# Performance work log

Measured on AMD Instinct MI355X. Metric: run time of the kernel, lower is better.

## Reference

```python
import math
import jax, jax.numpy as jnp
import numpy as np
from jax import lax

# Fixed values for the module's random shift hyperparams (in their legal ranges)
S2, S3, S5, S6 = 2, 1, -1, 1  # p_2_1_0, p_3_1_0, p_5_1_1, p_6_1_0


def setup_inputs() -> dict:
    key = jax.random.key(0)
    k1, k2, k3, k4, k5 = jax.random.split(key, 5)
    n, c, h, w = 16, 112, 48, 48
    x = jax.random.normal(k1, (n, c, h, w), dtype=jnp.float32)
    bound7 = math.sqrt(3.0 / (w * 3))
    p7_w = jax.random.uniform(k2, (3, w), minval=-bound7, maxval=bound7, dtype=jnp.float32)
    p8_w = jax.random.normal(k3, (1, c, h, 1), dtype=jnp.float32) * 0.02
    p19_w = jax.random.normal(k4, (1, c, 1, 1), dtype=jnp.float32) * 0.02
    cb = 1.0 / math.sqrt(c * 3)
    conv_w = jax.random.uniform(k5, (c, c, 1, 3), minval=-cb, maxval=cb, dtype=jnp.float32)
    return {"x": x, "p7_w": p7_w, "p8_w": p8_w, "p19_w": p19_w, "conv_w": conv_w}


def reference(x, p7_w, p8_w, p19_w, conv_w):
    n, c, h, w = x.shape
    hw = h * w
    # t_1: unfold (1,3) dilation (1,3) pad (0,3) -> width shifts of {-3,0,+3}, zero padded
    xp = jnp.pad(x, ((0, 0), (0, 0), (0, 0), (3, 3)))
    t1 = jnp.stack([xp[..., 3 * k: 3 * k + w] for k in range(3)], axis=2)  # (n,c,3,h,w)
    t2 = jnp.roll(x, S2, axis=2)
    t3 = jnp.roll(t1, S3, axis=3)
    t4 = t3.mean(axis=1)                     # (n,3,h,w)
    t5 = jnp.roll(t2, S5, axis=3)
    t6 = jnp.roll(t4, S6, axis=2)
    t7 = jnp.einsum('nkhw,kw->nh', t6, p7_w)  # einsum 'abcd,bdef->aecf' collapsed -> (n,h)
    t8 = p8_w * t5
    t9 = x + t8
    t10 = t8 - t9                             # mathematically -x, kept as written
    # p_11: Conv2d(c,c,(1,3),dilation=(1,2),padding=(0,2)), width-preserving
    t11 = lax.conv_general_dilated(
        t10, conv_w, window_strides=(1, 1), padding=((0, 0), (2, 2)),
        rhs_dilation=(1, 2), dimension_numbers=('NCHW', 'OIHW', 'NCHW'))
    # t_12: unfold (7,1) dilation (2,1) pad (6,0) on t_7 viewed (n,1,h,1)
    t7p = jnp.pad(t7, ((0, 0), (6, 6)))
    t12 = jnp.stack([t7p[:, 2 * k: 2 * k + h] for k in range(7)], axis=1)  # (n,7,h)
    t13 = jnp.maximum(t11, x)
    # t_14 = bmm(x^T, t13)/sqrt(c): (n,hw,hw)
    t14 = jnp.einsum('ncp,ncq->npq', x.reshape(n, c, hw), t13.reshape(n, c, hw)) / math.sqrt(c)
    t15 = jnp.abs(t12)
    t17 = t15.mean(axis=2)                    # (n,7)
    t18 = (t17[:, None, :] - t10.reshape(n, c * h * w // 7, 7)).reshape(n, c, h, w)
    t19 = p19_w * t18
    # t_16 = t7 - t14 (broadcast over last h*w*w of row-block view), t_20 = t7 + t16
    t14r = t14.reshape(n, h, w * h * w)
    t7b = t7[:, :, None]
    t16 = t7b - t14r
    t20 = (t7b + t16).reshape(n, hw, hw)
    t21 = jnp.einsum('ncp,npq->ncq', t19.reshape(n, c, hw), t20) / math.sqrt(hw)
    return t21.reshape(n, c, h, w)
```

## Files before the change

### kernel.cpp

```cpp
#include <hip/hip_runtime.h>

typedef __attribute__((ext_vector_type(8))) short bfrag;
typedef __attribute__((ext_vector_type(4))) float f32x4;

namespace {
constexpr int N_ = 16, C_ = 112, H_ = 48, W_ = 48, HW_ = 2304;
constexpr int NKS = 18;
constexpr int WS_T7 = 0;
constexpr int WS_A = 1024;
constexpr int WS_WPACK = 40960;
constexpr int WS_GBF = 62464;
constexpr int WS_SPART = 177152;
}

__device__ __forceinline__ float f4e(const float4& v, int e) {
  return e == 0 ? v.x : e == 1 ? v.y : e == 2 ? v.z : v.w;
}
__device__ __forceinline__ unsigned short f2bf(float f) {
  unsigned u = __float_as_uint(f);
  return (unsigned short)((u + 0x7FFFu + ((u >> 16) & 1u)) >> 16);
}
__device__ __forceinline__ float bf2f(unsigned short s) {
  return __uint_as_float(((unsigned)s) << 16);
}

__global__ __launch_bounds__(192) void ath_t7(const float* __restrict__ x,
                                              const float* __restrict__ p7,
                                              float* __restrict__ ws) {
  const int h = blockIdx.x, n = blockIdx.y;
  const int tid = threadIdx.x;
  __shared__ float q[48];
  __shared__ float wred[3];
  if (tid < 48) {
    float s = 0.f;
#pragma unroll
    for (int k = 0; k < 3; ++k) {
      int wp = tid + 3 - 3 * k;
      if (wp >= 0 && wp < 48) s += p7[k * 48 + wp];
    }
    q[tid] = s;
  }
  __syncthreads();
  const int c16 = tid / 12, qq = tid - 12 * c16;
  const float qv0 = q[4 * qq], qv1 = q[4 * qq + 1];
  const float qv2 = q[4 * qq + 2], qv3 = q[4 * qq + 3];
  float d = 0.f;
#pragma unroll
  for (int p = 0; p < 7; ++p) {
    const int c = c16 + 16 * p;
    float4 v = *(const float4*)&x[((size_t)n * C_ + c) * HW_ + h * W_ + 4 * qq];
    d += v.x * qv0 + v.y * qv1 + v.z * qv2 + v.w * qv3;
  }
#pragma unroll
  for (int off = 32; off >= 1; off >>= 1) d += __shfl_xor(d, off);
  if ((tid & 63) == 0) wred[tid >> 6] = d;
  __syncthreads();
  if (tid == 0)
    ws[WS_T7 + n * H_ + (h + 2) % 48] =
        (wred[0] + wred[1] + wred[2]) * (1.0f / 112.0f);
}

__global__ __launch_bounds__(256) void ath_gram(const float* __restrict__ x,
                                                const float* __restrict__ cw,
                                                float* __restrict__ ws) {
  const int bid = blockIdx.x;
  const int tid = threadIdx.x;
  if (bid >= 2 * NKS * N_) {
    int idx = (bid - 2 * NKS * N_) * 256 + tid;
    if (idx < 3 * 112 * 32) {
      int kx = idx / (112 * 32);
      int r = idx - kx * 112 * 32;
      int o = r >> 5;
      int i0 = (r & 31) * 4;
      unsigned short v[4];
#pragma unroll
      for (int e = 0; e < 4; ++e) {
        int i = i0 + e;
        v[e] = (i < 112) ? f2bf(cw[o * 336 + i * 3 + kx]) : (unsigned short)0;
      }
      unsigned short* wp = (unsigned short*)(ws + WS_WPACK);
      *(ushort4*)&wp[(kx * 112 + o) * 128 + i0] = make_ushort4(v[0], v[1], v[2], v[3]);
    }
    return;
  }
  const int half = bid & 1;
  const int ks = (bid >> 1) % NKS;
  const int n = bid / (2 * NKS);
  const int k0 = ks * 128;
  const int lane = tid & 63, wv = tid >> 6;
  const int lr = lane & 15, lg = lane >> 4;
  __shared__ __align__(16) unsigned short As[112][136];
  __shared__ __align__(16) unsigned short t7r[136];
  __shared__ float t7s[48];
  __shared__ float s17[8];
  if (tid < 48) t7s[tid] = ws[WS_T7 + n * H_ + tid];
  __syncthreads();
  if (tid < 7) {
    float s = 0.f;
    for (int hh = 0; hh < 48; ++hh) {
      int j = 2 * tid + hh - 6;
      if (j >= 0 && j < 48) s += fabsf(t7s[j]);
    }
    s17[tid] = s * (1.0f / 48.0f);
  }
  if (tid >= 64 && tid < 192) t7r[tid - 64] = f2bf(t7s[(k0 + tid - 64) / 48]);
  if (tid >= 192 && tid < 200) t7r[128 + (tid - 192)] = 0;
  const int ti = wv + 4 * half;
  bfrag breg[4];
  if (ti < 7) {
    const float* bp = &x[((size_t)n * C_ + 16 * ti + lr) * HW_ + k0 + 8 * lg];
#pragma unroll
    for (int kb = 0; kb < 4; ++kb) {
      float4 v0 = *(const float4*)(bp + 32 * kb);
      float4 v1 = *(const float4*)(bp + 32 * kb + 4);
      breg[kb][0] = (short)f2bf(v0.x); breg[kb][1] = (short)f2bf(v0.y);
      breg[kb][2] = (short)f2bf(v0.z); breg[kb][3] = (short)f2bf(v0.w);
      breg[kb][4] = (short)f2bf(v1.x); breg[kb][5] = (short)f2bf(v1.y);
      breg[kb][6] = (short)f2bf(v1.z); breg[kb][7] = (short)f2bf(v1.w);
    }
  }
  __syncthreads();
  const int kq = tid & 31, cg = tid >> 5;
  const int base7 = (k0 + 4 * kq) % 7;
#pragma unroll
  for (int r = 0; r < 14; ++r) {
    const int c = cg + 8 * r;
    float4 v = *(const float4*)&x[((size_t)n * C_ + c) * HW_ + k0 + 4 * kq];
    int cls0 = (base7 + c) % 7;
    unsigned short a4[4];
#pragma unroll
    for (int e = 0; e < 4; ++e) {
      int cl = cls0 + e;
      cl = (cl >= 7) ? cl - 7 : cl;
      a4[e] = f2bf(f4e(v, e) + s17[cl]);
    }
    *(ushort4*)&As[c][4 * kq] = make_ushort4(a4[0], a4[1], a4[2], a4[3]);
  }
  __syncthreads();
  if (ti == 7) {
    const bfrag zero8 = {0, 0, 0, 0, 0, 0, 0, 0};
#pragma unroll
    for (int kb = 0; kb < 4; ++kb)
      breg[kb] = (lr == 0) ? *(const bfrag*)&t7r[8 * lg + 32 * kb] : zero8;
  }
  f32x4 acc[7];
#pragma unroll
  for (int j = 0; j < 7; ++j) acc[j] = (f32x4){0.f, 0.f, 0.f, 0.f};
#pragma unroll
  for (int kb = 0; kb < 4; ++kb) {
#pragma unroll
    for (int tc = 0; tc < 7; ++tc) {
      bfrag a = *(const bfrag*)&As[16 * tc + lr][8 * lg + 32 * kb];
      acc[tc] = __builtin_amdgcn_mfma_f32_16x16x32_bf16(a, breg[kb], acc[tc], 0, 0, 0);
    }
  }
  float* sp = ws + WS_SPART + (size_t)(n * NKS + ks) * 14336;
#pragma unroll
  for (int tc = 0; tc < 7; ++tc)
#pragma unroll
    for (int e = 0; e < 4; ++e)
      sp[(16 * tc + 4 * lg + e) * 128 + 16 * ti + lr] = acc[tc][e];
}

__global__ __launch_bounds__(128) void ath_assemble(const float* __restrict__ p19,
                                                    float* __restrict__ ws) {
  const int bid = blockIdx.x;
  const int n = bid / 28, g = bid % 28;
  const int tid = threadIdx.x;
  const int cloc = tid >> 5, q = tid & 31;
  const int c = 4 * g + cloc;
  const int i0 = 4 * q;
  float4 s = make_float4(0.f, 0.f, 0.f, 0.f);
#pragma unroll
  for (int ks = 0; ks < NKS; ++ks) {
    float4 t = *(const float4*)&ws[WS_SPART + (size_t)(n * NKS + ks) * 14336 + c * 128 + i0];
    s.x += t.x; s.y += t.y; s.z += t.z; s.w += t.w;
  }
  unsigned short* gb = (unsigned short*)(ws + WS_GBF);
  if (i0 < 112) {
    const float scale = 1.0f / (48.0f * sqrtf(112.0f));
    const float pc = p19[c];
    *(ushort4*)&gb[((size_t)n * C_ + c) * 128 + i0] =
        make_ushort4(f2bf(pc * s.x * scale), f2bf(pc * s.y * scale),
                     f2bf(pc * s.z * scale), f2bf(pc * s.w * scale));
  } else {
    *(ushort4*)&gb[((size_t)n * C_ + c) * 128 + i0] = make_ushort4(0, 0, 0, 0);
    if (i0 == 112) ws[WS_A + n * C_ + c] = p19[c] * s.x * (2.0f / 48.0f);
  }
}

__global__ __launch_bounds__(256) void ath_fused(const float* __restrict__ x,
                                                 const float* __restrict__ ws,
                                                 float* __restrict__ out) {
  const int h = blockIdx.x, n = blockIdx.y;
  const int tid = threadIdx.x;
  const int lane = tid & 63, wv = tid >> 6;
  const int lr = lane & 15, lg = lane >> 4;
  __shared__ __align__(16) unsigned short xT[52][136];
  __shared__ __align__(16) unsigned short buf[112][136];
  __shared__ float sA[112];
  const float* xb = x + (size_t)n * C_ * HW_ + h * W_;
  const unsigned short* wp = (const unsigned short*)(ws + WS_WPACK);
  const unsigned short* gb = (const unsigned short*)(ws + WS_GBF) + (size_t)n * C_ * 128;
  for (int idx = tid; idx < 52 * 24; idx += 256) {
    int r2 = idx / 24, cc = 112 + idx % 24;
    xT[r2][cc] = 0;
  }
  for (int idx = tid; idx < 4 * 112; idx += 256) {
    int rr = idx / 112;
    int r2 = (rr < 2) ? rr : 48 + rr;
    xT[r2][idx % 112] = 0;
  }
  if (tid < 112) sA[tid] = ws[WS_A + n * C_ + tid];
  for (int idx = tid; idx < 672; idx += 256) {
    int i2 = idx / 12, q = idx - i2 * 12;
    float4 a = *(const float4*)&xb[(size_t)(2 * i2) * HW_ + 4 * q];
    float4 b = *(const float4*)&xb[(size_t)(2 * i2 + 1) * HW_ + 4 * q];
#pragma unroll
    for (int e = 0; e < 4; ++e) {
      unsigned pk = (unsigned)f2bf(f4e(a, e)) | ((unsigned)f2bf(f4e(b, e)) << 16);
      *(unsigned*)&xT[4 * q + 2 + e][2 * i2] = pk;
    }
  }
  for (int idx = tid; idx < 1792; idx += 256) {
    int row = idx >> 4, cq = idx & 15;
    *(float4*)&buf[row][cq * 8] = *(const float4*)&wp[(size_t)row * 128 + cq * 8];
  }
  __syncthreads();

  f32x4 acc[6];
#pragma unroll
  for (int j = 0; j < 6; ++j) acc[j] = (f32x4){0.f, 0.f, 0.f, 0.f};
  for (int kx = 0; kx < 3; ++kx) {
    if (kx) {
      __syncthreads();
      for (int idx = tid; idx < 1792; idx += 256) {
        int row = idx >> 4, cq = idx & 15;
        *(float4*)&buf[row][cq * 8] =
            *(const float4*)&wp[(size_t)(kx * 112 + row) * 128 + cq * 8];
      }
      __syncthreads();
    }
#pragma unroll
    for (int j = 0; j < 6; ++j) {
      int t = wv + 4 * j;
      if (t < 21) {
        int m = t / 3, nt = t - 3 * m;
        int o0 = m * 16, w0 = nt * 16;
#pragma unroll
        for (int kb = 0; kb < 4; ++kb) {
          bfrag a = *(const bfrag*)&buf[o0 + lr][8 * lg + 32 * kb];
          bfrag b = *(const bfrag*)&xT[w0 + lr + 2 * kx][8 * lg + 32 * kb];
          acc[j] = __builtin_amdgcn_mfma_f32_16x16x32_bf16(a, b, acc[j], 0, 0, 0);
        }
      }
    }
  }
  unsigned short tv[6][4];
#pragma unroll
  for (int j = 0; j < 6; ++j) {
    int t = wv + 4 * j;
    if (t < 21) {
      int m = t / 3, nt = t - 3 * m;
      int o0 = m * 16, w0 = nt * 16;
#pragma unroll
      for (int e = 0; e < 4; ++e) {
        float xv = bf2f(xT[w0 + lr + 2][o0 + 4 * lg + e]);
        tv[j][e] = f2bf(fmaxf(-acc[j][e], xv));
      }
    }
  }
  __syncthreads();
#pragma unroll
  for (int j = 0; j < 6; ++j) {
    int t = wv + 4 * j;
    if (t < 21) {
      int m = t / 3, nt = t - 3 * m;
      int o0 = m * 16, w0 = nt * 16;
      unsigned pk0 = (unsigned)tv[j][0] | ((unsigned)tv[j][1] << 16);
      unsigned pk1 = (unsigned)tv[j][2] | ((unsigned)tv[j][3] << 16);
      *(unsigned*)&xT[w0 + lr + 2][o0 + 4 * lg] = pk0;
      *(unsigned*)&xT[w0 + lr + 2][o0 + 4 * lg + 2] = pk1;
    }
  }
  for (int idx = tid; idx < 1792; idx += 256) {
    int row = idx >> 4, cq = idx & 15;
    *(float4*)&buf[row][cq * 8] = *(const float4*)&gb[(size_t)row * 128 + cq * 8];
  }
  __syncthreads();

#pragma unroll
  for (int j = 0; j < 6; ++j) {
    int t = wv + 4 * j;
    if (t < 21) {
      int m = t / 3, nt = t - 3 * m;
      int c0 = m * 16, w0 = nt * 16;
      f32x4 acc2 = {0.f, 0.f, 0.f, 0.f};
#pragma unroll
      for (int kb = 0; kb < 4; ++kb) {
        bfrag a = *(const bfrag*)&buf[c0 + lr][8 * lg + 32 * kb];
        bfrag b = *(const bfrag*)&xT[w0 + lr + 2][8 * lg + 32 * kb];
        acc2 = __builtin_amdgcn_mfma_f32_16x16x32_bf16(a, b, acc2, 0, 0, 0);
      }
#pragma unroll
      for (int e = 0; e < 4; ++e) {
        int c = c0 + 4 * lg + e;
        out[((size_t)n * C_ + c) * HW_ + h * W_ + w0 + lr] = sA[c] - acc2[e];
      }
    }
  }
}

extern "C" void kernel_launch(void* const* d_in, const int* in_sizes, int n_in,
                              void* d_out, int out_size, void* d_ws, size_t ws_size,
                              hipStream_t stream) {
  const float* x = (const float*)d_in[0];
  const float* p7 = (const float*)d_in[1];
  const float* p19 = (const float*)d_in[3];
  const float* cw = (const float*)d_in[4];
  float* ws = (float*)d_ws;
  float* out = (float*)d_out;

  ath_t7<<<dim3(H_, N_), 192, 0, stream>>>(x, p7, ws);
  ath_gram<<<2 * NKS * N_ + 42, 256, 0, stream>>>(x, cw, ws);
  ath_assemble<<<N_ * 28, 128, 0, stream>>>(p19, ws);
  ath_fused<<<dim3(H_, N_), 256, 0, stream>>>(x, ws, out);
}
```

Baseline: 46.64 us.

## Replace split-K partial buffers and assemble kernel with atomic accumulation

The gram kernel now adds its split-K partial results straight into a per-batch fp32 buffer with atomicAdd, instead of writing 18 separate partial slabs. The separate assemble reduction kernel is removed. The fused kernel now applies the p19 scale, does the bf16 conversion of the gram matrix, and computes the sA term itself. The accumulation buffer is zeroed inside the first kernel. This saves one launch and the partial-buffer traffic, at the cost of atomic contention on the shared buffer, extra conversion work in the fused kernel, and a summation order that is no longer deterministic.

```diff
diff --git a/kernel.cpp b/kernel.cpp
--- a/kernel.cpp
+++ b/kernel.cpp
@@ -7,18 +7,17 @@
 constexpr int N_ = 16, C_ = 112, H_ = 48, W_ = 48, HW_ = 2304;
 constexpr int NKS = 18;
 constexpr int WS_T7 = 0;
-constexpr int WS_A = 1024;
-constexpr int WS_WPACK = 40960;
-constexpr int WS_GBF = 62464;
-constexpr int WS_SPART = 177152;
+constexpr int WS_GF = 4096;
+constexpr int WS_WPACK = 233472;
+constexpr int GF_TOT = 229376;
 }
 
 __device__ __forceinline__ float f4e(const float4& v, int e) {
   return e == 0 ? v.x : e == 1 ? v.y : e == 2 ? v.z : v.w;
 }
-__device__ __forceinline__ unsigned short f2bf(float f) {
+__device__ __forceinline__ unsigned f2bf(float f) {
   unsigned u = __float_as_uint(f);
-  return (unsigned short)((u + 0x7FFFu + ((u >> 16) & 1u)) >> 16);
+  return (u + 0x7FFFu + ((u >> 16) & 1u)) >> 16;
 }
 __device__ __forceinline__ float bf2f(unsigned short s) {
   return __uint_as_float(((unsigned)s) << 16);
@@ -29,6 +28,10 @@
                                               float* __restrict__ ws) {
   const int h = blockIdx.x, n = blockIdx.y;
   const int tid = threadIdx.x;
+  {
+    int lb = (blockIdx.y * 48 + blockIdx.x) * 192 + tid;
+    for (int i = lb; i < GF_TOT; i += 768 * 192) ws[WS_GF + i] = 0.f;
+  }
   __shared__ float q[48];
   __shared__ float wred[3];
   if (tid < 48) {
@@ -76,7 +79,8 @@
 #pragma unroll
       for (int e = 0; e < 4; ++e) {
         int i = i0 + e;
-        v[e] = (i < 112) ? f2bf(cw[o * 336 + i * 3 + kx]) : (unsigned short)0;
+        v[e] = (i < 112) ? (unsigned short)f2bf(cw[o * 336 + i * 3 + kx])
+                         : (unsigned short)0;
       }
       unsigned short* wp = (unsigned short*)(ws + WS_WPACK);
       *(ushort4*)&wp[(kx * 112 + o) * 128 + i0] = make_ushort4(v[0], v[1], v[2], v[3]);
@@ -103,7 +107,8 @@
     }
     s17[tid] = s * (1.0f / 48.0f);
   }
-  if (tid >= 64 && tid < 192) t7r[tid - 64] = f2bf(t7s[(k0 + tid - 64) / 48]);
+  if (tid >= 64 && tid < 192)
+    t7r[tid - 64] = (unsigned short)f2bf(t7s[(k0 + tid - 64) / 48]);
   if (tid >= 192 && tid < 200) t7r[128 + (tid - 192)] = 0;
   const int ti = wv + 4 * half;
   bfrag breg[4];
@@ -120,11 +125,11 @@
     }
   }
   __syncthreads();
-  const int kq = tid & 31, cg = tid >> 5;
+  const int kq = tid & 31, cg2 = tid >> 5;
   const int base7 = (k0 + 4 * kq) % 7;
 #pragma unroll
   for (int r = 0; r < 14; ++r) {
-    const int c = cg + 8 * r;
+    const int c = cg2 + 8 * r;
     float4 v = *(const float4*)&x[((size_t)n * C_ + c) * HW_ + k0 + 4 * kq];
     int cls0 = (base7 + c) % 7;
     unsigned short a4[4];
@@ -132,7 +137,7 @@
     for (int e = 0; e < 4; ++e) {
       int cl = cls0 + e;
       cl = (cl >= 7) ? cl - 7 : cl;
-      a4[e] = f2bf(f4e(v, e) + s17[cl]);
+      a4[e] = (unsigned short)f2bf(f4e(v, e) + s17[cl]);
     }
     *(ushort4*)&As[c][4 * kq] = make_ushort4(a4[0], a4[1], a4[2], a4[3]);
   }
@@ -154,42 +159,16 @@
       acc[tc] = __builtin_amdgcn_mfma_f32_16x16x32_bf16(a, breg[kb], acc[tc], 0, 0, 0);
     }
   }
-  float* sp = ws + WS_SPART + (size_t)(n * NKS + ks) * 14336;
+  float* gf = ws + WS_GF + (size_t)n * 14336;
 #pragma unroll
   for (int tc = 0; tc < 7; ++tc)
 #pragma unroll
     for (int e = 0; e < 4; ++e)
-      sp[(16 * tc + 4 * lg + e) * 128 + 16 * ti + lr] = acc[tc][e];
-}
-
-__global__ __launch_bounds__(128) void ath_assemble(const float* __restrict__ p19,
-                                                    float* __restrict__ ws) {
-  const int bid = blockIdx.x;
-  const int n = bid / 28, g = bid % 28;
-  const int tid = threadIdx.x;
-  const int cloc = tid >> 5, q = tid & 31;
-  const int c = 4 * g + cloc;
-  const int i0 = 4 * q;
-  float4 s = make_float4(0.f, 0.f, 0.f, 0.f);
-#pragma unroll
-  for (int ks = 0; ks < NKS; ++ks) {
-    float4 t = *(const float4*)&ws[WS_SPART + (size_t)(n * NKS + ks) * 14336 + c * 128 + i0];
-    s.x += t.x; s.y += t.y; s.z += t.z; s.w += t.w;
-  }
-  unsigned short* gb = (unsigned short*)(ws + WS_GBF);
-  if (i0 < 112) {
-    const float scale = 1.0f / (48.0f * sqrtf(112.0f));
-    const float pc = p19[c];
-    *(ushort4*)&gb[((size_t)n * C_ + c) * 128 + i0] =
-        make_ushort4(f2bf(pc * s.x * scale), f2bf(pc * s.y * scale),
-                     f2bf(pc * s.z * scale), f2bf(pc * s.w * scale));
-  } else {
-    *(ushort4*)&gb[((size_t)n * C_ + c) * 128 + i0] = make_ushort4(0, 0, 0, 0);
-    if (i0 == 112) ws[WS_A + n * C_ + c] = p19[c] * s.x * (2.0f / 48.0f);
-  }
+      atomicAdd(&gf[(16 * tc + 4 * lg + e) * 128 + 16 * ti + lr], acc[tc][e]);
 }
 
 __global__ __launch_bounds__(256) void ath_fused(const float* __restrict__ x,
+                                                 const float* __restrict__ p19,
                                                  const float* __restrict__ ws,
                                                  float* __restrict__ out) {
   const int h = blockIdx.x, n = blockIdx.y;
@@ -199,9 +178,10 @@
   __shared__ __align__(16) unsigned short xT[52][136];
   __shared__ __align__(16) unsigned short buf[112][136];
   __shared__ float sA[112];
+  __shared__ float sP[112];
   const float* xb = x + (size_t)n * C_ * HW_ + h * W_;
   const unsigned short* wp = (const unsigned short*)(ws + WS_WPACK);
-  const unsigned short* gb = (const unsigned short*)(ws + WS_GBF) + (size_t)n * C_ * 128;
+  const float* gf = ws + WS_GF + (size_t)n * 14336;
   for (int idx = tid; idx < 52 * 24; idx += 256) {
     int r2 = idx / 24, cc = 112 + idx % 24;
     xT[r2][cc] = 0;
@@ -211,14 +191,19 @@
     int r2 = (rr < 2) ? rr : 48 + rr;
     xT[r2][idx % 112] = 0;
   }
-  if (tid < 112) sA[tid] = ws[WS_A + n * C_ + tid];
+  if (tid < 112) {
+    const float scale = 1.0f / (48.0f * sqrtf(112.0f));
+    float pc = p19[tid];
+    sA[tid] = pc * gf[tid * 128 + 112] * (2.0f / 48.0f);
+    sP[tid] = pc * scale;
+  }
   for (int idx = tid; idx < 672; idx += 256) {
     int i2 = idx / 12, q = idx - i2 * 12;
     float4 a = *(const float4*)&xb[(size_t)(2 * i2) * HW_ + 4 * q];
     float4 b = *(const float4*)&xb[(size_t)(2 * i2 + 1) * HW_ + 4 * q];
 #pragma unroll
     for (int e = 0; e < 4; ++e) {
-      unsigned pk = (unsigned)f2bf(f4e(a, e)) | ((unsigned)f2bf(f4e(b, e)) << 16);
+      unsigned pk = f2bf(f4e(a, e)) | (f2bf(f4e(b, e)) << 16);
       *(unsigned*)&xT[4 * q + 2 + e][2 * i2] = pk;
     }
   }
@@ -266,7 +251,7 @@
 #pragma unroll
       for (int e = 0; e < 4; ++e) {
         float xv = bf2f(xT[w0 + lr + 2][o0 + 4 * lg + e]);
-        tv[j][e] = f2bf(fmaxf(-acc[j][e], xv));
+        tv[j][e] = (unsigned short)f2bf(fmaxf(-acc[j][e], xv));
       }
     }
   }
@@ -285,7 +270,14 @@
   }
   for (int idx = tid; idx < 1792; idx += 256) {
     int row = idx >> 4, cq = idx & 15;
-    *(float4*)&buf[row][cq * 8] = *(const float4*)&gb[(size_t)row * 128 + cq * 8];
+    float4 a = *(const float4*)&gf[(size_t)row * 128 + cq * 8];
+    float4 b = *(const float4*)&gf[(size_t)row * 128 + cq * 8 + 4];
+    uint4 pk;
+    pk.x = f2bf(a.x) | (f2bf(a.y) << 16);
+    pk.y = f2bf(a.z) | (f2bf(a.w) << 16);
+    pk.z = f2bf(b.x) | (f2bf(b.y) << 16);
+    pk.w = f2bf(b.z) | (f2bf(b.w) << 16);
+    *(uint4*)&buf[row][cq * 8] = pk;
   }
   __syncthreads();
 
@@ -305,7 +297,8 @@
 #pragma unroll
       for (int e = 0; e < 4; ++e) {
         int c = c0 + 4 * lg + e;
-        out[((size_t)n * C_ + c) * HW_ + h * W_ + w0 + lr] = sA[c] - acc2[e];
+        out[((size_t)n * C_ + c) * HW_ + h * W_ + w0 + lr] =
+            sA[c] - sP[c] * acc2[e];
       }
     }
   }
@@ -323,6 +316,5 @@
 
   ath_t7<<<dim3(H_, N_), 192, 0, stream>>>(x, p7, ws);
   ath_gram<<<2 * NKS * N_ + 42, 256, 0, stream>>>(x, cw, ws);
-  ath_assemble<<<N_ * 28, 128, 0, stream>>>(p19, ws);
-  ath_fused<<<dim3(H_, N_), 256, 0, stream>>>(x, ws, out);
-}
+  ath_fused<<<dim3(H_, N_), 256, 0, stream>>>(x, p19, ws, out);
+}
```

New measurement: 51.87 us. 1.11x slower.
